# Kernel tuning notes

Measured on AMD Instinct MI355X. Metric: run time of the kernel, lower is better.

The kernel has to match this reference:

```python
import jax, jax.numpy as jnp
import numpy as np

N = 50000       # num nodes
F_NODE = 8      # node_features
T_IN = 8        # num_timestamps_in (A3TGCN periods)
T_OUT = 4       # num_timestamps_out
HID = 16        # A3TGCN out_channels (hard-coded in module)
E = 800000      # num edges


def setup_inputs() -> dict:
    key = jax.random.key(0)
    ks = jax.random.split(key, 12)
    f32 = jnp.float32
    x = jax.random.normal(ks[0], (N, F_NODE, T_IN), dtype=f32)
    edge_index = jax.random.randint(ks[1], (2, E), 0, N)

    def w(k, shape):
        return (jax.random.normal(k, shape, dtype=f32) * 0.1)

    return {
        "x": x,
        "edge_index": edge_index,
        "attention": w(ks[2], (T_IN,)),
        "Wz": w(ks[3], (F_NODE, HID)), "bz": jnp.zeros((HID,), f32),
        "Lz_w": w(ks[4], (2 * HID, HID)), "Lz_b": jnp.zeros((HID,), f32),
        "Wr": w(ks[5], (F_NODE, HID)), "br": jnp.zeros((HID,), f32),
        "Lr_w": w(ks[6], (2 * HID, HID)), "Lr_b": jnp.zeros((HID,), f32),
        "Wh": w(ks[7], (F_NODE, HID)), "bh": jnp.zeros((HID,), f32),
        "Lh_w": w(ks[8], (2 * HID, HID)), "Lh_b": jnp.zeros((HID,), f32),
        "W_out": w(ks[9], (HID, F_NODE)), "b_out": jnp.zeros((F_NODE,), f32),
    }


def _gcn_norms(src, dst):
    # PyG gcn_norm: add self loops (weight 1), symmetric D^-1/2 (A+I) D^-1/2
    deg = jax.ops.segment_sum(jnp.ones((E,), jnp.float32), dst, num_segments=N) + 1.0
    dinv = jax.lax.rsqrt(deg)
    return dinv[src] * dinv[dst], dinv * dinv  # per-edge norm, self-loop norm


def _gcn(X, W, b, src, dst, norm_e, norm_self):
    xw = X @ W                                        # [N, HID]
    agg = jax.ops.segment_sum(xw[src] * norm_e[:, None], dst, num_segments=N)
    return agg + norm_self[:, None] * xw + b


def reference(x, edge_index, attention,
              Wz, bz, Lz_w, Lz_b,
              Wr, br, Lr_w, Lr_b,
              Wh, bh, Lh_w, Lh_b,
              W_out, b_out):
    src, dst = edge_index[0], edge_index[1]
    norm_e, norm_self = _gcn_norms(src, dst)
    probs = jax.nn.softmax(attention)                 # attention over periods

    def tgcn_cell(Xp, H):
        # GRU with GCNConv-based gates (TGCN)
        Z = jax.nn.sigmoid(
            jnp.concatenate([_gcn(Xp, Wz, bz, src, dst, norm_e, norm_self), H], axis=1) @ Lz_w + Lz_b)
        R = jax.nn.sigmoid(
            jnp.concatenate([_gcn(Xp, Wr, br, src, dst, norm_e, norm_self), H], axis=1) @ Lr_w + Lr_b)
        H_t = jnp.tanh(
            jnp.concatenate([_gcn(Xp, Wh, bh, src, dst, norm_e, norm_self), H * R], axis=1) @ Lh_w + Lh_b)
        return Z * H + (1.0 - Z) * H_t

    def a3tgcn(x_cur):
        xs = jnp.transpose(x_cur, (2, 0, 1))          # [T_IN, N, F]
        def step(carry, inp):
            H, H_acc = carry
            Xp, p = inp
            H = tgcn_cell(Xp, H)
            return (H, H_acc + p * H), None
        init = (jnp.zeros((N, HID), x_cur.dtype), jnp.zeros((N, HID), x_cur.dtype))
        (_, H_acc), _ = jax.lax.scan(step, init, (xs, probs))
        return H_acc

    outs = []
    for _ in range(T_OUT):
        h = jax.nn.relu(a3tgcn(x)) @ W_out + b_out    # [N, F]
        h = h[:, :, None]                              # [N, F, 1]
        x = jnp.concatenate([x[:, :, 1:], h], axis=2)  # slide window
        outs.append(h)
    return jnp.concatenate(outs, axis=2)               # [N, F, T_OUT]
```

## Files before the change

kernel.cpp:

```cpp
#include <hip/hip_runtime.h>

#define NN 50000
#define NE 800000
#define N8 (8*NN)
#define CAP 64

__device__ __forceinline__ float sigmoidf_(float x){ return 1.0f/(1.0f+__expf(-x)); }
__device__ __forceinline__ float tanhfast_(float x){ return 1.0f - 2.0f/(__expf(2.0f*x)+1.0f); }

__global__ void k_zero_fold(int* __restrict__ cnt, const float* __restrict__ att,
    const float* __restrict__ Wz, const float* __restrict__ bz,
    const float* __restrict__ Lzw, const float* __restrict__ Lzb,
    const float* __restrict__ Wr, const float* __restrict__ br,
    const float* __restrict__ Lrw, const float* __restrict__ Lrb,
    const float* __restrict__ Wh, const float* __restrict__ bh,
    const float* __restrict__ Lhw, const float* __restrict__ Lhb,
    const float* __restrict__ Wo, const float* __restrict__ bo,
    float* __restrict__ fold){
    if(blockIdx.x < 196){
        cnt[blockIdx.x*256 + threadIdx.x] = 0;
        return;
    }
    int tid = threadIdx.x;
    const float* Ws[3]  = {Wz, Wr, Wh};
    const float* bs[3]  = {bz, br, bh};
    const float* Ls[3]  = {Lzw, Lrw, Lhw};
    const float* Lbs[3] = {Lzb, Lrb, Lhb};
    if(tid < 48){
        int g = tid >> 4, j = tid & 15;
        const float* W = Ws[g]; const float* L = Ls[g];
        float c = Lbs[g][j];
        for(int k = 0; k < 16; ++k) c += bs[g][k] * L[k*16 + j];
        fold[1280 + g*16 + j] = c;
        for(int f = 0; f < 8; ++f){
            float m = 0.f;
            for(int k = 0; k < 16; ++k) m += W[f*16 + k] * L[k*16 + j];
            fold[j*28 + g*8 + f] = m;
        }
    }
    for(int idx = tid; idx < 768; idx += 256){
        int g = idx >> 8, rr = idx & 255, i = rr >> 4, j = rr & 15;
        fold[448 + j*52 + g*16 + i] = Ls[g][(16 + i)*16 + j];
    }
    for(int idx = tid; idx < 128; idx += 256) fold[1328 + idx] = Wo[idx];
    if(tid < 8) fold[1456 + tid] = bo[tid];
    if(tid == 0){
        float mx = att[0];
        for(int k = 1; k < 8; ++k) mx = fmaxf(mx, att[k]);
        float den = 0.f, ex[8];
        for(int k = 0; k < 8; ++k){ ex[k] = __expf(att[k] - mx); den += ex[k]; }
        for(int k = 0; k < 8; ++k) fold[1464 + k] = ex[k] / den;
    }
}

__global__ void k_build(const int* __restrict__ ei, int* __restrict__ cnt,
                        int* __restrict__ csr){
    int e = blockIdx.x*256 + threadIdx.x;
    int s = ei[e], d = ei[NE + e];
    int r = atomicAdd(&cnt[d], 1);
    if(r < CAP) csr[(size_t)d*CAP + r] = s;
}

__global__ void k_xscale(const float* __restrict__ x, const int* __restrict__ cnt,
                         float* __restrict__ xs){
    int idx = blockIdx.x*256 + threadIdx.x;
    int n = idx >> 4;
    const float4* x4 = (const float4*)x;
    float4 v = x4[idx];
    float d = rsqrtf((float)cnt[n] + 1.0f);
    v.x *= d; v.y *= d; v.z *= d; v.w *= d;
    ((float4*)xs)[idx] = v;
}

__global__ __launch_bounds__(256) void k_gather_x2(
    const int* __restrict__ cnt, const int* __restrict__ csr,
    const float* __restrict__ xs, float* __restrict__ Pall){
    int lane = threadIdx.x & 63;
    int n = blockIdx.x*4 + (threadIdx.x >> 6);
    int g = lane >> 4;
    int q = lane & 15;
    int cn = cnt[n];
    int deg = cn < CAP ? cn : CAP;
    const int* row = csr + (size_t)n*CAP;
    const float4* xs4 = (const float4*)xs;

    float4 a0, a1, a2, a3;
    if(g == 0){ a0 = xs4[(size_t)n*16 + q]; }
    else      { a0.x = a0.y = a0.z = a0.w = 0.f; }
    a1.x = a1.y = a1.z = a1.w = 0.f;
    a2 = a1; a3 = a1;

    int it = 0;
    for(; it + 16 <= deg; it += 16){
        int ka = it + g;
        int s0 = row[ka], s1 = row[ka+4], s2 = row[ka+8], s3 = row[ka+12];
        float4 v0 = xs4[(size_t)s0*16 + q];
        float4 v1 = xs4[(size_t)s1*16 + q];
        float4 v2 = xs4[(size_t)s2*16 + q];
        float4 v3 = xs4[(size_t)s3*16 + q];
        a0.x += v0.x; a0.y += v0.y; a0.z += v0.z; a0.w += v0.w;
        a1.x += v1.x; a1.y += v1.y; a1.z += v1.z; a1.w += v1.w;
        a2.x += v2.x; a2.y += v2.y; a2.z += v2.z; a2.w += v2.w;
        a3.x += v3.x; a3.y += v3.y; a3.z += v3.z; a3.w += v3.w;
    }
    for(int k = it + g; k < deg; k += 4){
        float4 v = xs4[(size_t)row[k]*16 + q];
        a0.x += v.x; a0.y += v.y; a0.z += v.z; a0.w += v.w;
    }
    a0.x += a1.x + a2.x + a3.x;
    a0.y += a1.y + a2.y + a3.y;
    a0.z += a1.z + a2.z + a3.z;
    a0.w += a1.w + a2.w + a3.w;

    a0.x += __shfl_xor(a0.x, 16); a0.y += __shfl_xor(a0.y, 16);
    a0.z += __shfl_xor(a0.z, 16); a0.w += __shfl_xor(a0.w, 16);
    a0.x += __shfl_xor(a0.x, 32); a0.y += __shfl_xor(a0.y, 32);
    a0.z += __shfl_xor(a0.z, 32); a0.w += __shfl_xor(a0.w, 32);

    if(g == 0){
        float dn = rsqrtf((float)cn + 1.0f);
        float a[4] = {a0.x, a0.y, a0.z, a0.w};
        #pragma unroll
        for(int m = 0; m < 4; ++m){
            int r = q*4 + m;
            int f = r >> 3, t = r & 7;
            Pall[(size_t)t*N8 + n*8 + f] = dn * a[m];
        }
    }
}

template<int TOUT>
__global__ __launch_bounds__(256) void k_cell_t(
    const float* __restrict__ Pall, float* __restrict__ Ph_all,
    const float* __restrict__ fold, const int* __restrict__ cnt,
    const int* __restrict__ csr, float* __restrict__ out,
    const float* __restrict__ hs_in, float* __restrict__ hs_out){
    __shared__ float s[1472];
    __shared__ float xch[256];
    for(int k = threadIdx.x; k < 1472; k += 256) s[k] = fold[k];
    __syncthreads();

    int tid = threadIdx.x;
    int j = tid & 15;
    int nb = tid & 240;
    int n = blockIdx.x*16 + (tid >> 4);
    int cn = cnt[n];
    float dn = rsqrtf((float)cn + 1.0f);

    float ub[8][8];
    #pragma unroll
    for(int st = 0; st < 8; ++st){
        if(TOUT > 0 && st == 7) continue;
        const int t = TOUT + st;
        const float* base = (t < 8) ? (Pall + (size_t)t*N8)
                                    : (Ph_all + (size_t)(t - 8)*N8);
        const float4* p = (const float4*)(base + (size_t)n*8);
        float4 b0 = p[0], b1 = p[1];
        ub[st][0]=b0.x; ub[st][1]=b0.y; ub[st][2]=b0.z; ub[st][3]=b0.w;
        ub[st][4]=b1.x; ub[st][5]=b1.y; ub[st][6]=b1.z; ub[st][7]=b1.w;
    }

    if(TOUT > 0){
        int f = j & 7, g = j >> 3;
        int deg = cn < CAP ? cn : CAP;
        const int* row = csr + (size_t)n*CAP;
        float ga = 0.f, gb = 0.f;
        int k = g;
        for(; k + 4 <= deg; k += 4){
            ga += hs_in[row[k]*8 + f];
            gb += hs_in[row[k+2]*8 + f];
        }
        if(k < deg){ ga += hs_in[row[k]*8 + f]; k += 2; }
        if(k < deg){ gb += hs_in[row[k]*8 + f]; }
        ga += gb;
        ga += __shfl_xor(ga, 8);
        float uh = dn * (ga + hs_in[n*8 + f]);
        if(j < 8){
            xch[nb + j] = uh;
            Ph_all[(size_t)(TOUT-1)*N8 + n*8 + j] = uh;
        }
        *(float4*)&ub[7][0] = *(const float4*)&xch[nb + 0];
        *(float4*)&ub[7][4] = *(const float4*)&xch[nb + 4];
    }

    const float* Mrow = s + j*28;
    const float* Lrow = s + 448 + j*52;
    float mw[24];
    #pragma unroll
    for(int k = 0; k < 6; ++k) *(float4*)&mw[k*4] = *(const float4*)&Mrow[k*4];
    float lw[48];
    #pragma unroll
    for(int k = 0; k < 12; ++k) *(float4*)&lw[k*4] = *(const float4*)&Lrow[k*4];
    float cz = s[1280 + j], cr = s[1296 + j], ch = s[1312 + j];

    float Hown = 0.f, Acc = 0.f;

    #pragma unroll
    for(int st = 0; st < 8; ++st){
        const float* u = ub[st];

        float Hf[16];
        xch[tid] = Hown;
        *(float4*)&Hf[0]  = *(const float4*)&xch[nb + 0];
        *(float4*)&Hf[4]  = *(const float4*)&xch[nb + 4];
        *(float4*)&Hf[8]  = *(const float4*)&xch[nb + 8];
        *(float4*)&Hf[12] = *(const float4*)&xch[nb + 12];

        float az = cz, ar = cr;
        #pragma unroll
        for(int f = 0; f < 8; ++f){ az += u[f]*mw[f]; ar += u[f]*mw[8+f]; }
        #pragma unroll
        for(int i = 0; i < 16; ++i){ az += Hf[i]*lw[i]; ar += Hf[i]*lw[16+i]; }
        float Z = sigmoidf_(az);
        float R = sigmoidf_(ar);

        float HRf[16];
        xch[tid] = Hown*R;
        *(float4*)&HRf[0]  = *(const float4*)&xch[nb + 0];
        *(float4*)&HRf[4]  = *(const float4*)&xch[nb + 4];
        *(float4*)&HRf[8]  = *(const float4*)&xch[nb + 8];
        *(float4*)&HRf[12] = *(const float4*)&xch[nb + 12];

        float ah = ch;
        #pragma unroll
        for(int f = 0; f < 8; ++f) ah += u[f]*mw[16+f];
        #pragma unroll
        for(int i = 0; i < 16; ++i) ah += HRf[i]*lw[32+i];
        float ht = tanhfast_(ah);
        Hown = Z*Hown + (1.0f - Z)*ht;
        Acc += s[1464 + st]*Hown;
    }

    float rf[16];
    xch[tid] = Acc > 0.f ? Acc : 0.f;
    *(float4*)&rf[0]  = *(const float4*)&xch[nb + 0];
    *(float4*)&rf[4]  = *(const float4*)&xch[nb + 4];
    *(float4*)&rf[8]  = *(const float4*)&xch[nb + 8];
    *(float4*)&rf[12] = *(const float4*)&xch[nb + 12];
    if(j < 8){
        int f = j;
        float o = s[1456 + f];
        #pragma unroll
        for(int jj = 0; jj < 16; ++jj) o += rf[jj] * s[1328 + jj*8 + f];
        out[(size_t)n*32 + f*4 + TOUT] = o;
        if(TOUT < 3) hs_out[n*8 + f] = dn * o;
    }
}

extern "C" void kernel_launch(void* const* d_in, const int* in_sizes, int n_in,
                              void* d_out, int out_size, void* d_ws, size_t ws_size,
                              hipStream_t stream){
    const float* x   = (const float*)d_in[0];
    const int*   ei  = (const int*)  d_in[1];
    const float* att = (const float*)d_in[2];
    const float* Wz  = (const float*)d_in[3];  const float* bz  = (const float*)d_in[4];
    const float* Lzw = (const float*)d_in[5];  const float* Lzb = (const float*)d_in[6];
    const float* Wr  = (const float*)d_in[7];  const float* br  = (const float*)d_in[8];
    const float* Lrw = (const float*)d_in[9];  const float* Lrb = (const float*)d_in[10];
    const float* Wh  = (const float*)d_in[11]; const float* bh  = (const float*)d_in[12];
    const float* Lhw = (const float*)d_in[13]; const float* Lhb = (const float*)d_in[14];
    const float* Wo  = (const float*)d_in[15]; const float* bo  = (const float*)d_in[16];
    float* out = (float*)d_out;

    char* w = (char*)d_ws;
    int*   cnt  = (int*)  (w);
    int*   csr  = (int*)  (w + (size_t)50176*4);
    float* fold = (float*)(w + (size_t)3250176*4);
    float* xs   = (float*)(w + (size_t)3251712*4);
    float* Pall = (float*)(w + (size_t)6451712*4);
    float* Ph   = xs;
    float* hs0  = xs + 1200000;
    float* hs1  = xs + 1600000;

    dim3 b(256);
    k_zero_fold<<<197, b, 0, stream>>>(cnt, att, Wz, bz, Lzw, Lzb, Wr, br, Lrw, Lrb,
                                       Wh, bh, Lhw, Lhb, Wo, bo, fold);
    k_build<<<3125, b, 0, stream>>>(ei, cnt, csr);
    k_xscale<<<3125, b, 0, stream>>>(x, cnt, xs);
    k_gather_x2<<<12500, b, 0, stream>>>(cnt, csr, xs, Pall);

    k_cell_t<0><<<3125, b, 0, stream>>>(Pall, Ph, fold, cnt, csr, out, hs1, hs0);
    k_cell_t<1><<<3125, b, 0, stream>>>(Pall, Ph, fold, cnt, csr, out, hs0, hs1);
    k_cell_t<2><<<3125, b, 0, stream>>>(Pall, Ph, fold, cnt, csr, out, hs1, hs0);
    k_cell_t<3><<<3125, b, 0, stream>>>(Pall, Ph, fold, cnt, csr, out, hs0, hs1);
}
```

Baseline: 307.0 us.

## Store CSR indices as 16-bit and fold source scaling into gather

After: 305.6 us. Within noise of the previous version (-0.5%).

```diff
diff --git a/kernel.cpp b/kernel.cpp
--- a/kernel.cpp
+++ b/kernel.cpp
@@ -54,39 +54,31 @@
 }
 
 __global__ void k_build(const int* __restrict__ ei, int* __restrict__ cnt,
-                        int* __restrict__ csr){
+                        unsigned short* __restrict__ csr){
     int e = blockIdx.x*256 + threadIdx.x;
     int s = ei[e], d = ei[NE + e];
     int r = atomicAdd(&cnt[d], 1);
-    if(r < CAP) csr[(size_t)d*CAP + r] = s;
-}
-
-__global__ void k_xscale(const float* __restrict__ x, const int* __restrict__ cnt,
-                         float* __restrict__ xs){
-    int idx = blockIdx.x*256 + threadIdx.x;
-    int n = idx >> 4;
-    const float4* x4 = (const float4*)x;
-    float4 v = x4[idx];
-    float d = rsqrtf((float)cnt[n] + 1.0f);
-    v.x *= d; v.y *= d; v.z *= d; v.w *= d;
-    ((float4*)xs)[idx] = v;
+    if(r < CAP) csr[(size_t)d*CAP + r] = (unsigned short)s;
 }
 
 __global__ __launch_bounds__(256) void k_gather_x2(
-    const int* __restrict__ cnt, const int* __restrict__ csr,
-    const float* __restrict__ xs, float* __restrict__ Pall){
+    const int* __restrict__ cnt, const unsigned short* __restrict__ csr,
+    const float* __restrict__ x, float* __restrict__ Pall){
     int lane = threadIdx.x & 63;
     int n = blockIdx.x*4 + (threadIdx.x >> 6);
     int g = lane >> 4;
     int q = lane & 15;
     int cn = cnt[n];
     int deg = cn < CAP ? cn : CAP;
-    const int* row = csr + (size_t)n*CAP;
-    const float4* xs4 = (const float4*)xs;
+    const unsigned short* row = csr + (size_t)n*CAP;
+    const float4* x4 = (const float4*)x;
+    float dn = rsqrtf((float)cn + 1.0f);
 
     float4 a0, a1, a2, a3;
-    if(g == 0){ a0 = xs4[(size_t)n*16 + q]; }
-    else      { a0.x = a0.y = a0.z = a0.w = 0.f; }
+    if(g == 0){
+        float4 v = x4[(size_t)n*16 + q];
+        a0.x = dn*v.x; a0.y = dn*v.y; a0.z = dn*v.z; a0.w = dn*v.w;
+    } else { a0.x = a0.y = a0.z = a0.w = 0.f; }
     a1.x = a1.y = a1.z = a1.w = 0.f;
     a2 = a1; a3 = a1;
 
@@ -94,18 +86,24 @@
     for(; it + 16 <= deg; it += 16){
         int ka = it + g;
         int s0 = row[ka], s1 = row[ka+4], s2 = row[ka+8], s3 = row[ka+12];
-        float4 v0 = xs4[(size_t)s0*16 + q];
-        float4 v1 = xs4[(size_t)s1*16 + q];
-        float4 v2 = xs4[(size_t)s2*16 + q];
-        float4 v3 = xs4[(size_t)s3*16 + q];
-        a0.x += v0.x; a0.y += v0.y; a0.z += v0.z; a0.w += v0.w;
-        a1.x += v1.x; a1.y += v1.y; a1.z += v1.z; a1.w += v1.w;
-        a2.x += v2.x; a2.y += v2.y; a2.z += v2.z; a2.w += v2.w;
-        a3.x += v3.x; a3.y += v3.y; a3.z += v3.z; a3.w += v3.w;
+        float d0 = rsqrtf((float)cnt[s0] + 1.0f);
+        float d1 = rsqrtf((float)cnt[s1] + 1.0f);
+        float d2 = rsqrtf((float)cnt[s2] + 1.0f);
+        float d3 = rsqrtf((float)cnt[s3] + 1.0f);
+        float4 v0 = x4[(size_t)s0*16 + q];
+        float4 v1 = x4[(size_t)s1*16 + q];
+        float4 v2 = x4[(size_t)s2*16 + q];
+        float4 v3 = x4[(size_t)s3*16 + q];
+        a0.x += d0*v0.x; a0.y += d0*v0.y; a0.z += d0*v0.z; a0.w += d0*v0.w;
+        a1.x += d1*v1.x; a1.y += d1*v1.y; a1.z += d1*v1.z; a1.w += d1*v1.w;
+        a2.x += d2*v2.x; a2.y += d2*v2.y; a2.z += d2*v2.z; a2.w += d2*v2.w;
+        a3.x += d3*v3.x; a3.y += d3*v3.y; a3.z += d3*v3.z; a3.w += d3*v3.w;
     }
     for(int k = it + g; k < deg; k += 4){
-        float4 v = xs4[(size_t)row[k]*16 + q];
-        a0.x += v.x; a0.y += v.y; a0.z += v.z; a0.w += v.w;
+        int s0 = row[k];
+        float d0 = rsqrtf((float)cnt[s0] + 1.0f);
+        float4 v = x4[(size_t)s0*16 + q];
+        a0.x += d0*v.x; a0.y += d0*v.y; a0.z += d0*v.z; a0.w += d0*v.w;
     }
     a0.x += a1.x + a2.x + a3.x;
     a0.y += a1.y + a2.y + a3.y;
@@ -118,7 +116,6 @@
     a0.z += __shfl_xor(a0.z, 32); a0.w += __shfl_xor(a0.w, 32);
 
     if(g == 0){
-        float dn = rsqrtf((float)cn + 1.0f);
         float a[4] = {a0.x, a0.y, a0.z, a0.w};
         #pragma unroll
         for(int m = 0; m < 4; ++m){
@@ -133,7 +130,7 @@
 __global__ __launch_bounds__(256) void k_cell_t(
     const float* __restrict__ Pall, float* __restrict__ Ph_all,
     const float* __restrict__ fold, const int* __restrict__ cnt,
-    const int* __restrict__ csr, float* __restrict__ out,
+    const unsigned short* __restrict__ csr, float* __restrict__ out,
     const float* __restrict__ hs_in, float* __restrict__ hs_out){
     __shared__ float s[1472];
     __shared__ float xch[256];
@@ -163,7 +160,7 @@
     if(TOUT > 0){
         int f = j & 7, g = j >> 3;
         int deg = cn < CAP ? cn : CAP;
-        const int* row = csr + (size_t)n*CAP;
+        const unsigned short* row = csr + (size_t)n*CAP;
         float ga = 0.f, gb = 0.f;
         int k = g;
         for(; k + 4 <= deg; k += 4){
@@ -263,21 +260,19 @@
     float* out = (float*)d_out;
 
     char* w = (char*)d_ws;
-    int*   cnt  = (int*)  (w);
-    int*   csr  = (int*)  (w + (size_t)50176*4);
-    float* fold = (float*)(w + (size_t)3250176*4);
-    float* xs   = (float*)(w + (size_t)3251712*4);
-    float* Pall = (float*)(w + (size_t)6451712*4);
-    float* Ph   = xs;
-    float* hs0  = xs + 1200000;
-    float* hs1  = xs + 1600000;
+    int*            cnt  = (int*)           (w);
+    unsigned short* csr  = (unsigned short*)(w + (size_t)50176*4);
+    float*          fold = (float*)         (w + (size_t)1650176*4);
+    float*          Ph   = (float*)         (w + (size_t)1651712*4);
+    float*          hs0  = (float*)         (w + (size_t)2851712*4);
+    float*          hs1  = (float*)         (w + (size_t)3251712*4);
+    float*          Pall = (float*)         (w + (size_t)3651712*4);
 
     dim3 b(256);
     k_zero_fold<<<197, b, 0, stream>>>(cnt, att, Wz, bz, Lzw, Lzb, Wr, br, Lrw, Lrb,
                                        Wh, bh, Lhw, Lhb, Wo, bo, fold);
     k_build<<<3125, b, 0, stream>>>(ei, cnt, csr);
-    k_xscale<<<3125, b, 0, stream>>>(x, cnt, xs);
-    k_gather_x2<<<12500, b, 0, stream>>>(cnt, csr, xs, Pall);
+    k_gather_x2<<<12500, b, 0, stream>>>(cnt, csr, x, Pall);
 
     k_cell_t<0><<<3125, b, 0, stream>>>(Pall, Ph, fold, cnt, csr, out, hs1, hs0);
     k_cell_t<1><<<3125, b, 0, stream>>>(Pall, Ph, fold, cnt, csr, out, hs0, hs1);
```
